# Performance work log

Hardware: AMD Instinct MI355X
Metric: run time of the kernel (lower is better)

The kernel has to match this reference:

```python
import jax, jax.numpy as jnp
import numpy as np

NEG_SLOPE = 0.2  # self.alpha


def setup_inputs() -> dict:
    key = jax.random.key(0)
    k1, k2, k3, k4 = jax.random.split(key, 4)
    N, E, in_dim, out_dim = 50000, 800000, 128, 64
    inp = jax.random.normal(k1, (N, in_dim), dtype=jnp.float32)
    edge = jax.random.randint(k2, (2, E), 0, N, dtype=jnp.int64)
    # xavier_normal init scales
    W = jax.random.normal(k3, (in_dim, out_dim), dtype=jnp.float32) * np.sqrt(2.0 / (in_dim + out_dim))
    a = jax.random.normal(k4, (2 * out_dim, 1), dtype=jnp.float32) * np.sqrt(2.0 / (2 * out_dim + 1))
    return {"input": inp, "edge": edge, "W": W, "a": a}


def reference(input, edge, W, a):
    # eval mode: dropout is a no-op
    N = input.shape[0]
    h = input @ W                           # [N, out_dim]
    src, dst = edge[0], edge[1]             # [E], [E]
    out_dim = h.shape[1]
    a_src, a_dst = a[:out_dim, 0], a[out_dim:, 0]
    # equivalent to cat([h[src], h[dst]], 1) @ a, without materializing [E, 2*out_dim]
    score = (h @ a_src)[src] + (h @ a_dst)[dst]          # [E]
    e = jax.nn.leaky_relu(score, negative_slope=NEG_SLOPE)
    # sparse softmax over each row (segment by src)
    m = jax.ops.segment_max(e, src, num_segments=N)      # [N], -inf for empty rows
    m = jnp.where(jnp.isfinite(m), m, 0.0)
    ex = jnp.exp(e - m[src])                             # [E]
    s = jax.ops.segment_sum(ex, src, num_segments=N)     # [N]
    attn = ex / s[src]                                   # [E]
    # scatter-aggregate: out[i] = sum_{(i,j) in E} attn_ij * h[j]
    out = jax.ops.segment_sum(attn[:, None] * h[dst], src, num_segments=N)  # [N, out_dim]
    return jax.nn.elu(out)
```

## Files before the change

kernel.cpp:

```cpp
#include <hip/hip_runtime.h>
#include <hip/hip_fp16.h>
#include <math.h>

#define IN_DIM 128
#define OUT_DIM 64
#define NEG_SLOPE 0.2f

#define BUCKET_SRCS 32
#define CAP 1024
#define MAXBK 2048

#define KC 32
#define TROWS 128

__global__ __launch_bounds__(256) void gemm_hs_hd(
    const float* __restrict__ in, const float* __restrict__ W,
    const float* __restrict__ a, __half* __restrict__ hb,
    float* __restrict__ hs, float* __restrict__ hd,
    int* __restrict__ zero_base, int zero_n, int N)
{
    __shared__ float At[KC][TROWS + 4];
    __shared__ float Wl[KC][OUT_DIM];

    const int t  = threadIdx.x;
    for (int i = blockIdx.x * 256 + t; i < zero_n; i += gridDim.x * 256)
        zero_base[i] = 0;

    const int tx = t & 15;
    const int ty = t >> 4;
    const int r0 = blockIdx.x * TROWS;

    float acc[8][4];
    #pragma unroll
    for (int i = 0; i < 8; ++i)
        #pragma unroll
        for (int j = 0; j < 4; ++j) acc[i][j] = 0.f;

    for (int kc = 0; kc < IN_DIM / KC; ++kc) {
        const int k0 = kc * KC;
        __syncthreads();
        {
            const int kq = (t & 7) * 4;
            const int rl0 = t >> 3;
            #pragma unroll
            for (int p = 0; p < 4; ++p) {
                int rl = p * 32 + rl0;
                int row = r0 + rl; if (row >= N) row = N - 1;
                float4 v = *(const float4*)&in[(size_t)row * IN_DIM + k0 + kq];
                At[kq + 0][rl] = v.x;
                At[kq + 1][rl] = v.y;
                At[kq + 2][rl] = v.z;
                At[kq + 3][rl] = v.w;
            }
        }
        {
            const int c4 = (t & 15) * 4;
            const int kl0 = t >> 4;
            #pragma unroll
            for (int p = 0; p < 2; ++p) {
                int kl = p * 16 + kl0;
                *(float4*)&Wl[kl][c4] = *(const float4*)&W[(size_t)(k0 + kl) * OUT_DIM + c4];
            }
        }
        __syncthreads();

        #pragma unroll 4
        for (int k = 0; k < KC; ++k) {
            float4 a0 = *(const float4*)&At[k][ty * 8];
            float4 a1 = *(const float4*)&At[k][ty * 8 + 4];
            float4 b0 = *(const float4*)&Wl[k][tx * 4];
            float av[8] = {a0.x, a0.y, a0.z, a0.w, a1.x, a1.y, a1.z, a1.w};
            float bv[4] = {b0.x, b0.y, b0.z, b0.w};
            #pragma unroll
            for (int i = 0; i < 8; ++i)
                #pragma unroll
                for (int j = 0; j < 4; ++j)
                    acc[i][j] = fmaf(av[i], bv[j], acc[i][j]);
        }
    }

    float4 as = *(const float4*)&a[tx * 4];
    float4 ad = *(const float4*)&a[OUT_DIM + tx * 4];
    float asv[4] = {as.x, as.y, as.z, as.w};
    float adv[4] = {ad.x, ad.y, ad.z, ad.w};

    #pragma unroll
    for (int i = 0; i < 8; ++i) {
        int row = r0 + ty * 8 + i;
        float ps = 0.f, pd = 0.f;
        #pragma unroll
        for (int j = 0; j < 4; ++j) {
            ps = fmaf(acc[i][j], asv[j], ps);
            pd = fmaf(acc[i][j], adv[j], pd);
        }
        #pragma unroll
        for (int off = 1; off < 16; off <<= 1) {
            ps += __shfl_xor(ps, off, 64);
            pd += __shfl_xor(pd, off, 64);
        }
        if (row < N) {
            union { __half2 h2[2]; uint2 u; } cv;
            cv.h2[0] = __floats2half2_rn(acc[i][0], acc[i][1]);
            cv.h2[1] = __floats2half2_rn(acc[i][2], acc[i][3]);
            *(uint2*)&hb[(size_t)row * OUT_DIM + tx * 4] = cv.u;
            if (tx == 0) { hs[row] = ps; hd[row] = pd; }
        }
    }
}

#define PA_CHUNK 4096
__global__ __launch_bounds__(256) void partition_kernel(
    const int* __restrict__ src, const int* __restrict__ dst,
    int* __restrict__ gcursor, int* __restrict__ pairbuf, int E, int NBK)
{
    __shared__ int lcount[MAXBK];
    __shared__ int lbase[MAXBK];
    __shared__ int lrun[MAXBK];
    const int t = threadIdx.x;
    for (int i = t; i < NBK; i += 256) lcount[i] = 0;
    __syncthreads();

    const int base = blockIdx.x * PA_CHUNK;
    int pk[16], b[16];
    int nloc = 0;
    #pragma unroll
    for (int j = 0; j < 16; ++j) {
        int i = base + j * 256 + t;
        if (i < E) {
            int s = src[i];
            b[j]  = s >> 5;
            pk[j] = ((s & 31) << 16) | dst[i];
            atomicAdd(&lcount[b[j]], 1);
            nloc = j + 1;
        }
    }
    __syncthreads();
    for (int i = t; i < NBK; i += 256) {
        int c = lcount[i];
        int gb = 0;
        if (c > 0) gb = atomicAdd(&gcursor[i], c);
        lbase[i] = i * CAP + gb;
        lrun[i] = 0;
    }
    __syncthreads();
    for (int j = 0; j < nloc; ++j) {
        int r = atomicAdd(&lrun[b[j]], 1);
        int pos = lbase[b[j]] + r;
        if (pos - b[j] * CAP < CAP)
            pairbuf[pos] = pk[j];
    }
}

__global__ __launch_bounds__(256) void node_kernel(
    const __half* __restrict__ hb, const float* __restrict__ hs,
    const float* __restrict__ hd, const int* __restrict__ gcursor,
    const int* __restrict__ pairbuf, float* __restrict__ out, int N)
{
    __shared__ int2  spair[CAP];
    __shared__ float ssums[BUCKET_SRCS];
    __shared__ float hsl[BUCKET_SRCS];
    __shared__ int   cnt[BUCKET_SRCS];
    __shared__ int   excl[BUCKET_SRCS];
    __shared__ int   lcur[BUCKET_SRCS];

    const int t = threadIdx.x;
    const int b = blockIdx.x;
    const int M = min(gcursor[b], CAP);

    if (t < BUCKET_SRCS) {
        int node = b * BUCKET_SRCS + t;
        hsl[t] = (node < N) ? hs[node] : 0.f;
        cnt[t] = 0;
        ssums[t] = 0.f;
    }
    __syncthreads();

    int   dloc[CAP / 256], slv[CAP / 256];
    float exv[CAP / 256];
    int nl = 0;
    #pragma unroll
    for (int j = 0; j < CAP / 256; ++j) {
        int i = j * 256 + t;
        if (i < M) {
            int pk = pairbuf[b * CAP + i];
            int sl = (pk >> 16) & 31;
            int d  = pk & 0xffff;
            float e = hsl[sl] + hd[d];
            e = (e >= 0.f) ? e : NEG_SLOPE * e;
            float ex = __expf(e);
            atomicAdd(&cnt[sl], 1);
            atomicAdd(&ssums[sl], ex);
            dloc[j] = d; slv[j] = sl; exv[j] = ex;
            nl = j + 1;
        }
    }
    __syncthreads();
    if (t < BUCKET_SRCS) {
        int raw = cnt[t];
        int v = raw;
        #pragma unroll
        for (int off = 1; off < BUCKET_SRCS; off <<= 1) {
            int u = __shfl_up(v, off, 64);
            if (t >= off) v += u;
        }
        excl[t] = v - raw;
        lcur[t] = v - raw;
    }
    __syncthreads();
    for (int j = 0; j < nl; ++j) {
        int r = atomicAdd(&lcur[slv[j]], 1);
        spair[r] = make_int2(__float_as_int(exv[j]), dloc[j]);
    }
    __syncthreads();

    const int lane = t & 63;
    const int wave = t >> 6;
    const int slot = lane >> 3;
    const int c8   = lane & 7;
    const int loc  = wave * 8 + slot;
    const int node = b * BUCKET_SRCS + loc;
    const bool valid = node < N;

    const int deg = cnt[loc];
    const int beg = excl[loc];
    const float inv = (valid && deg > 0) ? 1.f / ssums[loc] : 0.f;

    int dmax = deg;
    #pragma unroll
    for (int off = 8; off < 64; off <<= 1)
        dmax = max(dmax, __shfl_xor(dmax, off, 64));

    float acc[8];
    #pragma unroll
    for (int q = 0; q < 8; ++q) acc[q] = 0.f;

    for (int j = 0; j < dmax; ++j) {
        bool act = j < deg;
        int2 pr = spair[beg + (act ? j : 0)];
        float ex = act ? __int_as_float(pr.x) : 0.f;
        union { uint4 u; __half2 h2[4]; } hv;
        hv.u = *(const uint4*)&hb[(size_t)pr.y * OUT_DIM + c8 * 8];
        #pragma unroll
        for (int q = 0; q < 4; ++q) {
            acc[2 * q]     = fmaf(ex, __low2float(hv.h2[q]),  acc[2 * q]);
            acc[2 * q + 1] = fmaf(ex, __high2float(hv.h2[q]), acc[2 * q + 1]);
        }
    }

    if (valid) {
        float o[8];
        #pragma unroll
        for (int q = 0; q < 8; ++q) {
            float v = acc[q] * inv;
            o[q] = (v > 0.f) ? v : (__expf(v) - 1.f);
        }
        float4 o0 = {o[0], o[1], o[2], o[3]};
        float4 o1 = {o[4], o[5], o[6], o[7]};
        *(float4*)&out[(size_t)node * OUT_DIM + c8 * 8] = o0;
        *(float4*)&out[(size_t)node * OUT_DIM + c8 * 8 + 4] = o1;
    }
}

extern "C" void kernel_launch(void* const* d_in, const int* in_sizes, int n_in,
                              void* d_out, int out_size, void* d_ws, size_t ws_size,
                              hipStream_t stream)
{
    const float* input = (const float*)d_in[0];
    const int*   edge  = (const int*)d_in[1];
    const float* W     = (const float*)d_in[2];
    const float* a     = (const float*)d_in[3];
    float* out = (float*)d_out;

    const int N = in_sizes[0] / IN_DIM;
    const int E = in_sizes[1] / 2;
    const int* src = edge;
    const int* dst = edge + E;

    const int NBK = (N + BUCKET_SRCS - 1) / BUCKET_SRCS;

    size_t idx = 0;
    int* gcursor = (int*)d_ws + idx; idx += MAXBK;
    int* pairbuf = (int*)d_ws + idx; idx += (size_t)NBK * CAP;
    __half* hb = (__half*)((int*)d_ws + idx); idx += (size_t)N * OUT_DIM / 2;
    float* hs = (float*)((int*)d_ws + idx); idx += N;
    float* hd = (float*)((int*)d_ws + idx); idx += N;

    gemm_hs_hd<<<(N + TROWS - 1) / TROWS, 256, 0, stream>>>(
        input, W, a, hb, hs, hd, gcursor, NBK, N);
    partition_kernel<<<(E + PA_CHUNK - 1) / PA_CHUNK, 256, 0, stream>>>(
        src, dst, gcursor, pairbuf, E, NBK);
    node_kernel<<<NBK, 256, 0, stream>>>(hb, hs, hd, gcursor, pairbuf, out, N);
}
```

Before: 128.3 us.

## Compute node projection GEMM with fp16 MFMA instead of fp32 FMA

```diff
diff --git a/kernel.cpp b/kernel.cpp
--- a/kernel.cpp
+++ b/kernel.cpp
@@ -10,8 +10,10 @@
 #define CAP 1024
 #define MAXBK 2048
 
-#define KC 32
-#define TROWS 128
+typedef _Float16 half8 __attribute__((ext_vector_type(8)));
+typedef float floatx4 __attribute__((ext_vector_type(4)));
+
+#define GR 64
 
 __global__ __launch_bounds__(256) void gemm_hs_hd(
     const float* __restrict__ in, const float* __restrict__ W,
@@ -19,91 +21,100 @@
     float* __restrict__ hs, float* __restrict__ hd,
     int* __restrict__ zero_base, int zero_n, int N)
 {
-    __shared__ float At[KC][TROWS + 4];
-    __shared__ float Wl[KC][OUT_DIM];
-
-    const int t  = threadIdx.x;
+    __shared__ _Float16 Al[GR][IN_DIM];
+    __shared__ _Float16 Wt[OUT_DIM][IN_DIM + 8];
+    __shared__ _Float16 Crep[GR][OUT_DIM + 8];
+
+    const int t = threadIdx.x;
     for (int i = blockIdx.x * 256 + t; i < zero_n; i += gridDim.x * 256)
         zero_base[i] = 0;
 
-    const int tx = t & 15;
-    const int ty = t >> 4;
-    const int r0 = blockIdx.x * TROWS;
-
-    float acc[8][4];
-    #pragma unroll
-    for (int i = 0; i < 8; ++i)
-        #pragma unroll
-        for (int j = 0; j < 4; ++j) acc[i][j] = 0.f;
-
-    for (int kc = 0; kc < IN_DIM / KC; ++kc) {
-        const int k0 = kc * KC;
-        __syncthreads();
-        {
-            const int kq = (t & 7) * 4;
-            const int rl0 = t >> 3;
-            #pragma unroll
-            for (int p = 0; p < 4; ++p) {
-                int rl = p * 32 + rl0;
-                int row = r0 + rl; if (row >= N) row = N - 1;
-                float4 v = *(const float4*)&in[(size_t)row * IN_DIM + k0 + kq];
-                At[kq + 0][rl] = v.x;
-                At[kq + 1][rl] = v.y;
-                At[kq + 2][rl] = v.z;
-                At[kq + 3][rl] = v.w;
-            }
-        }
-        {
-            const int c4 = (t & 15) * 4;
-            const int kl0 = t >> 4;
-            #pragma unroll
-            for (int p = 0; p < 2; ++p) {
-                int kl = p * 16 + kl0;
-                *(float4*)&Wl[kl][c4] = *(const float4*)&W[(size_t)(k0 + kl) * OUT_DIM + c4];
-            }
-        }
-        __syncthreads();
-
-        #pragma unroll 4
-        for (int k = 0; k < KC; ++k) {
-            float4 a0 = *(const float4*)&At[k][ty * 8];
-            float4 a1 = *(const float4*)&At[k][ty * 8 + 4];
-            float4 b0 = *(const float4*)&Wl[k][tx * 4];
-            float av[8] = {a0.x, a0.y, a0.z, a0.w, a1.x, a1.y, a1.z, a1.w};
-            float bv[4] = {b0.x, b0.y, b0.z, b0.w};
-            #pragma unroll
-            for (int i = 0; i < 8; ++i)
-                #pragma unroll
-                for (int j = 0; j < 4; ++j)
-                    acc[i][j] = fmaf(av[i], bv[j], acc[i][j]);
-        }
-    }
-
-    float4 as = *(const float4*)&a[tx * 4];
-    float4 ad = *(const float4*)&a[OUT_DIM + tx * 4];
-    float asv[4] = {as.x, as.y, as.z, as.w};
-    float adv[4] = {ad.x, ad.y, ad.z, ad.w};
+    const int r0 = blockIdx.x * GR;
 
     #pragma unroll
     for (int i = 0; i < 8; ++i) {
-        int row = r0 + ty * 8 + i;
+        int q = i * 256 + t;
+        int row = q >> 5;
+        int kq  = (q & 31) * 4;
+        int grow = r0 + row; if (grow >= N) grow = N - 1;
+        float4 v = *(const float4*)&in[(size_t)grow * IN_DIM + kq];
+        union { __half2 h2[2]; uint2 u; } cv;
+        cv.h2[0] = __floats2half2_rn(v.x, v.y);
+        cv.h2[1] = __floats2half2_rn(v.z, v.w);
+        *(uint2*)&Al[row][kq] = cv.u;
+    }
+    #pragma unroll
+    for (int i = 0; i < 8; ++i) {
+        int q = i * 256 + t;
+        int k  = q >> 4;
+        int n4 = (q & 15) * 4;
+        float4 v = *(const float4*)&W[(size_t)k * OUT_DIM + n4];
+        Wt[n4 + 0][k] = (_Float16)v.x;
+        Wt[n4 + 1][k] = (_Float16)v.y;
+        Wt[n4 + 2][k] = (_Float16)v.z;
+        Wt[n4 + 3][k] = (_Float16)v.w;
+    }
+    __syncthreads();
+
+    const int lane = t & 63;
+    const int wave = t >> 6;
+    const int m16  = lane & 15;
+    const int quad = lane >> 4;
+
+    floatx4 acc[4];
+    #pragma unroll
+    for (int nt = 0; nt < 4; ++nt) acc[nt] = (floatx4){0.f, 0.f, 0.f, 0.f};
+
+    #pragma unroll
+    for (int kc = 0; kc < 4; ++kc) {
+        half8 af = *(const half8*)&Al[wave * 16 + m16][kc * 32 + quad * 8];
+        #pragma unroll
+        for (int nt = 0; nt < 4; ++nt) {
+            half8 bf = *(const half8*)&Wt[nt * 16 + m16][kc * 32 + quad * 8];
+            acc[nt] = __builtin_amdgcn_mfma_f32_16x16x32_f16(af, bf, acc[nt], 0, 0, 0);
+        }
+    }
+
+    float asl[4], adl[4];
+    #pragma unroll
+    for (int nt = 0; nt < 4; ++nt) {
+        asl[nt] = a[nt * 16 + m16];
+        adl[nt] = a[OUT_DIM + nt * 16 + m16];
+    }
+    #pragma unroll
+    for (int r = 0; r < 4; ++r) {
         float ps = 0.f, pd = 0.f;
         #pragma unroll
-        for (int j = 0; j < 4; ++j) {
-            ps = fmaf(acc[i][j], asv[j], ps);
-            pd = fmaf(acc[i][j], adv[j], pd);
+        for (int nt = 0; nt < 4; ++nt) {
+            ps = fmaf(acc[nt][r], asl[nt], ps);
+            pd = fmaf(acc[nt][r], adl[nt], pd);
         }
         #pragma unroll
         for (int off = 1; off < 16; off <<= 1) {
             ps += __shfl_xor(ps, off, 64);
             pd += __shfl_xor(pd, off, 64);
         }
-        if (row < N) {
-            union { __half2 h2[2]; uint2 u; } cv;
-            cv.h2[0] = __floats2half2_rn(acc[i][0], acc[i][1]);
-            cv.h2[1] = __floats2half2_rn(acc[i][2], acc[i][3]);
-            *(uint2*)&hb[(size_t)row * OUT_DIM + tx * 4] = cv.u;
-            if (tx == 0) { hs[row] = ps; hd[row] = pd; }
+        if (m16 == 0) {
+            int row = r0 + wave * 16 + quad * 4 + r;
+            if (row < N) { hs[row] = ps; hd[row] = pd; }
+        }
+    }
+
+    #pragma unroll
+    for (int nt = 0; nt < 4; ++nt)
+        #pragma unroll
+        for (int r = 0; r < 4; ++r)
+            Crep[wave * 16 + quad * 4 + r][nt * 16 + m16] = (_Float16)acc[nt][r];
+    __syncthreads();
+    #pragma unroll
+    for (int i = 0; i < 2; ++i) {
+        int idx = i * 256 + t;
+        int row = idx >> 3;
+        int seg = idx & 7;
+        int grow = r0 + row;
+        if (grow < N) {
+            uint4 v = *(const uint4*)&Crep[row][seg * 8];
+            *(uint4*)&hb[(size_t)grow * OUT_DIM + seg * 8] = v;
         }
     }
 }
@@ -285,7 +296,7 @@
     float* hs = (float*)((int*)d_ws + idx); idx += N;
     float* hd = (float*)((int*)d_ws + idx); idx += N;
 
-    gemm_hs_hd<<<(N + TROWS - 1) / TROWS, 256, 0, stream>>>(
+    gemm_hs_hd<<<(N + GR - 1) / GR, 256, 0, stream>>>(
         input, W, a, hb, hs, hd, gcursor, NBK, N);
     partition_kernel<<<(E + PA_CHUNK - 1) / PA_CHUNK, 256, 0, stream>>>(
         src, dst, gcursor, pairbuf, E, NBK);
```

After: 121.4 us. -5.4%, faster.
